# Kernel tuning notes

Hardware: AMD Instinct MI355X
Metric: run time of the kernel (lower is better)

Reference implementation:

```python
import jax, jax.numpy as jnp
import numpy as np

B, T, S = 64, 4096, 128


def setup_inputs() -> dict:
    key = jax.random.key(0)
    k1, k2 = jax.random.split(key)
    log_observation = jax.random.normal(k1, (B, T, S), dtype=jnp.float32)
    # a valid log-transition matrix (rows = from-state), all entries finite
    log_transition = jax.nn.log_softmax(jax.random.normal(k2, (S, S), dtype=jnp.float32), axis=1)
    return {"log_observation": log_observation, "log_transition": log_transition}


def reference(log_observation, log_transition):
    """CRF partition function (neg_log_likelihood_batch): -logsumexp over all paths.

    log_observation: [B, T, S], log_transition: [S, S] (from-state x to-state).
    Returns [B] negative log partition values.
    """
    obs_t = jnp.swapaxes(log_observation, 0, 1)  # [T, B, S] time-major for scan
    fv0 = obs_t[0]  # [B, S]

    def step(fv, obs):
        # (logsumexp, +) semiring recurrence: fv'[b,j] = LSE_i(fv[b,i] + A[i,j]) + obs[b,j]
        fv = jax.nn.logsumexp(fv[:, :, None] + log_transition[None], axis=1) + obs
        return fv, None

    fv, _ = jax.lax.scan(step, fv0, obs_t[1:])
    return -jax.nn.logsumexp(fv, axis=1)  # [B]
```

## Files before the change

kernel.cpp:

```cpp
#include <hip/hip_runtime.h>

typedef _Float16 half_t;
typedef _Float16 h8 __attribute__((ext_vector_type(8)));
typedef _Float16 h2 __attribute__((ext_vector_type(2)));
typedef float f4 __attribute__((ext_vector_type(4)));
typedef unsigned int uint32;
typedef unsigned long long u64;
typedef unsigned int u2v __attribute__((ext_vector_type(2)));

#define SHIFT16 2.772588722239781f
#define SHIFT8  2.0794415416798357f
#define WX 0
#define WQ 8192
#define WSC 16384
#define FAST_WS_BYTES 114688u

#define WAIT_VM(n)   asm volatile("s_waitcnt vmcnt(" #n ")" ::: "memory")

#define GL4(dst, addr, OFFSTR) \
    asm volatile("global_load_dwordx4 %0, %1, off offset:" OFFSTR \
                 : "=v"(dst) : "v"(addr))

__device__ __forceinline__ h2 pkrtz(float a, float b) {
    return __builtin_bit_cast(h2, __builtin_amdgcn_cvt_pkrtz(a, b));
}

__device__ __forceinline__ void swap32(uint32& a, uint32& b) {
#if __has_builtin(__builtin_amdgcn_permlane32_swap)
    u2v r = __builtin_amdgcn_permlane32_swap(a, b, false, false);
    a = r.x; b = r.y;
#else
    const uint32 pa = (uint32)__shfl_xor((int)a, 32);
    const uint32 pb = (uint32)__shfl_xor((int)b, 32);
    const bool hi = (threadIdx.x & 32) != 0;
    const uint32 na = hi ? pb : a;
    const uint32 nb = hi ? b : pa;
    a = na; b = nb;
#endif
}
__device__ __forceinline__ void swap16(uint32& a, uint32& b) {
#if __has_builtin(__builtin_amdgcn_permlane16_swap)
    u2v r = __builtin_amdgcn_permlane16_swap(a, b, false, false);
    a = r.x; b = r.y;
#else
    const uint32 sa = (uint32)__builtin_amdgcn_ds_swizzle((int)a, 0x401F);
    const uint32 sb = (uint32)__builtin_amdgcn_ds_swizzle((int)b, 0x401F);
    const bool m = (threadIdx.x & 16) != 0;
    const uint32 na = m ? sb : a;
    const uint32 nb = m ? b : sa;
    a = na; b = nb;
#endif
}

__device__ __forceinline__ float wavemax_hi(float M) {
    uint32 ma = __builtin_bit_cast(uint32, M), mb = ma;
    swap16(ma, mb);
    M = fmaxf(__builtin_bit_cast(float, ma), __builtin_bit_cast(float, mb));
    ma = __builtin_bit_cast(uint32, M); mb = ma;
    swap32(ma, mb);
    return fmaxf(__builtin_bit_cast(float, ma), __builtin_bit_cast(float, mb));
}

__device__ __forceinline__ float wavesum_hi(float S) {
    uint32 a = __builtin_bit_cast(uint32, S), b = a;
    swap16(a, b);
    S = __builtin_bit_cast(float, a) + __builtin_bit_cast(float, b);
    a = __builtin_bit_cast(uint32, S); b = a;
    swap32(a, b);
    return __builtin_bit_cast(float, a) + __builtin_bit_cast(float, b);
}

__device__ __forceinline__ float chain_sum(const f4 (&D)[8]) {
    f4 s4 = (D[0] + D[1]) + (D[2] + D[3]);
    s4 = s4 + ((D[4] + D[5]) + (D[6] + D[7]));
    float S = (s4.x + s4.y) + (s4.z + s4.w);
    return wavesum_hi(S);
}


#define TE(N) (FW ? (N) : (4095 - (N)))
#define WSEG 32
#define LSEG 64
#define NSEG 32

template <bool FW, int ST>
__device__ __forceinline__ void cstep(int v, int nv, bool head,
                                      f4 (&D)[8], const uint32 (&ep)[16],
                                      const h8 (&Af)[8][4],
                                      float& Lacc, float& rs, float& saK)
{
    const f4 Z = {0.f, 0.f, 0.f, 0.f};

    if (ST == 0) {
        #pragma unroll
        for (int mt = 0; mt < 8; ++mt) D[mt] = D[mt] * rs;
        if (v == WSEG) {
            if (head) {
                #pragma unroll
                for (int mt = 0; mt < 8; ++mt) D[mt] = (f4){1.f, 1.f, 1.f, 1.f};
            } else {
                saK = chain_sum(D);
            }
            Lacc = 0.f;
        }
    }
    if (ST == 3) {
        if (v != nv - 1) {
            f4 m01 = __builtin_elementwise_max(D[0], D[1]);
            f4 m23 = __builtin_elementwise_max(D[2], D[3]);
            f4 m45 = __builtin_elementwise_max(D[4], D[5]);
            f4 m67 = __builtin_elementwise_max(D[6], D[7]);
            f4 ma = __builtin_elementwise_max(
                        __builtin_elementwise_max(m01, m23),
                        __builtin_elementwise_max(m45, m67));
            float M = fmaxf(fmaxf(ma.x, ma.y), fmaxf(ma.z, ma.w));
            M = wavemax_hi(M);
            Lacc += __logf(M);
            rs = __builtin_amdgcn_rcpf(M);
        }
    }

    uint32 Wx[8], Wy[8];
    #pragma unroll
    for (int mt = 0; mt < 8; ++mt) {
        h2 w0 = pkrtz(D[mt].x, D[mt].y) * __builtin_bit_cast(h2, ep[2 * mt]);
        h2 w1 = pkrtz(D[mt].z, D[mt].w) * __builtin_bit_cast(h2, ep[2 * mt + 1]);
        Wx[mt] = __builtin_bit_cast(uint32, w0);
        Wy[mt] = __builtin_bit_cast(uint32, w1);
    }

    h8 Bf[4];
    #pragma unroll
    for (int kc = 0; kc < 4; ++kc) {
        uint32 x0 = Wx[2 * kc], x1 = Wx[2 * kc + 1];
        uint32 y0 = Wy[2 * kc], y1 = Wy[2 * kc + 1];
        swap32(x0, x1); swap16(x0, x1);
        swap32(y0, y1); swap16(y0, y1);
        uint4 bv; bv.x = x0; bv.y = y0; bv.z = x1; bv.w = y1;
        Bf[kc] = __builtin_bit_cast(h8, bv);
    }

    #pragma unroll
    for (int mt = 0; mt < 8; ++mt) {
        f4 acc = Z;
        acc = __builtin_amdgcn_mfma_f32_16x16x32_f16(Af[mt][0], Bf[0], acc, 0, 0, 0);
        acc = __builtin_amdgcn_mfma_f32_16x16x32_f16(Af[mt][1], Bf[1], acc, 0, 0, 0);
        acc = __builtin_amdgcn_mfma_f32_16x16x32_f16(Af[mt][2], Bf[2], acc, 0, 0, 0);
        acc = __builtin_amdgcn_mfma_f32_16x16x32_f16(Af[mt][3], Bf[3], acc, 0, 0, 0);
        D[mt] = acc;
    }
}

#define ISSUE8(B, IPE) do {                                                   \
    int ip_ = (IPE);                                                          \
    ip_ = ip_ < 0 ? 0 : (ip_ > NITd - 1 ? NITd - 1 : ip_);                    \
    const u64 a_ = lbase + ((u64)TE(ip_) << 9);                               \
    GL4(G[B][0], a_, "0");   GL4(G[B][1], a_, "64");                          \
    GL4(G[B][2], a_, "128"); GL4(G[B][3], a_, "192");                         \
    GL4(G[B][4], a_, "256"); GL4(G[B][5], a_, "320");                         \
    GL4(G[B][6], a_, "384"); GL4(G[B][7], a_, "448");                        \
} while (0)

#define SUBSTEP(U)  do {                                                      \
    const int v_ = tt * 8 + (U);                                              \
    if (v_ < nv) {                                                            \
        ISSUE8(((U) + 3) & 3, itb + v_ + 3);                                  \
        WAIT_VM(24);                             \
        __builtin_amdgcn_sched_barrier(0);                                    \
        uint32 ep[16];                                                        \
        _Pragma("unroll")                                                     \
        for (int mt = 0; mt < 8; ++mt) {                                      \
            const f4 ov = __builtin_bit_cast(f4, G[(U) & 3][mt]);             \
            ep[2 * mt] = __builtin_bit_cast(uint32,                           \
                pkrtz(__expf(ov.x - SHIFT16), __expf(ov.y - SHIFT16)));       \
            ep[2 * mt + 1] = __builtin_bit_cast(uint32,                       \
                pkrtz(__expf(ov.z - SHIFT16), __expf(ov.w - SHIFT16)));       \
        }                                                                     \
        cstep<FW, (U) & 3>(v_, nv, head, D, ep, Af, Lacc, rs, saK);           \
    } } while (0)

template <bool FW>
__device__ __forceinline__ void chain(const float* __restrict__ obs,
                                      const float* __restrict__ trans,
                                      float* __restrict__ ws, int cg, int sg)
{
    const int l = threadIdx.x & 63;
    const int q = l >> 4, n = l & 15;
    const int NITd = FW ? 2048 : 2047;
    const int nv   = (!FW && sg == NSEG - 1) ? (WSEG + LSEG - 1) : (WSEG + LSEG);
    const bool head = (sg == 0);
    const bool last = (sg == NSEG - 1);
    const int itb = sg * LSEG - WSEG;
    const u64 lbase = (u64)(const char*)obs
                    + ((u64)(cg * 16 + n) << 21)
                    + (u64)(q << 4);

    h8 Af[8][4];
    #pragma unroll
    for (int mt = 0; mt < 8; ++mt)
        #pragma unroll
        for (int kc = 0; kc < 4; ++kc) {
            h8 a;
            #pragma unroll
            for (int j = 0; j < 8; ++j) {
                const int k = kc * 32 + q * 8 + j;
                const int m = mt * 16 + n;
                a[j] = (half_t)__expf(FW ? trans[k * 128 + m] : trans[m * 128 + k]);
            }
            Af[mt][kc] = a;
        }

    uint4 G[4][8];
    ISSUE8(0, itb + 0);
    ISSUE8(1, itb + 1);
    ISSUE8(2, itb + 2);

    f4 D[8];
    #pragma unroll
    for (int mt = 0; mt < 8; ++mt) D[mt] = (f4){1.f, 1.f, 1.f, 1.f};
    float Lacc = 0.f, rs = 1.f, saK = 1.f;

    #pragma unroll 1
    for (int tt = 0; tt < (WSEG + LSEG) / 8; ++tt) {
        SUBSTEP(0); SUBSTEP(1); SUBSTEP(2); SUBSTEP(3);
        SUBSTEP(4); SUBSTEP(5); SUBSTEP(6); SUBSTEP(7);
    }
    WAIT_VM(0);

    const float swK = chain_sum(D);
    if (last) {
        float* Xo = ws + (FW ? WX : WQ) + ((cg * 16 + n) << 7);
        #pragma unroll
        for (int mt = 0; mt < 8; ++mt)
            *(f4*)&Xo[mt * 16 + q * 4] = D[mt];
    }
    float* sc = ws + WSC + (cg * 2 + (FW ? 0 : 1)) * 1536;
    if (q == 0) {
        sc[sg * 16 + n]        = Lacc;
        sc[512 + sg * 16 + n]  = swK;
        sc[1024 + sg * 16 + n] = head ? 1.0f : saK;
    }
}

__global__ __launch_bounds__(64, 1)
void crf_mfma(const float* __restrict__ obs, const float* __restrict__ trans,
              float* __restrict__ ws)
{
    const int bid = blockIdx.x;
    const int g = bid & 7;
    const int sg = bid >> 3;
    const int cg = g & 3;
    if (g < 4) chain<true >(obs, trans, ws, cg, sg);
    else       chain<false>(obs, trans, ws, cg, sg);
}

__global__ __launch_bounds__(64)
void crf_comb(const float* __restrict__ obs, const float* __restrict__ ws,
              float* __restrict__ out)
{
    const int b = blockIdx.x, l = threadIdx.x;
    const int cg = b >> 4, n = b & 15;
    const int s0 = 2 * l;
    const float2 o = *(const float2*)&obs[((((size_t)b << 12) + 2048) << 7) + s0];
    const float e0 = __expf(o.x - SHIFT16), e1 = __expf(o.y - SHIFT16);
    float v = ws[WX + b * 128 + s0] * e0 * ws[WQ + b * 128 + s0]
            + ws[WX + b * 128 + s0 + 1] * e1 * ws[WQ + b * 128 + s0 + 1];

    const int dir = l >> 5, s = l & 31;
    const float* sc = ws + WSC + (cg * 2 + dir) * 1536;
    float corr = sc[s * 16 + n];
    if (s >= 1)
        corr += __logf(sc[512 + (s - 1) * 16 + n])
              - __logf(sc[1024 + s * 16 + n]);

    v += __shfl_xor(v, 1);  v += __shfl_xor(v, 2);  v += __shfl_xor(v, 4);
    v += __shfl_xor(v, 8);  v += __shfl_xor(v, 16); v += __shfl_xor(v, 32);
    corr += __shfl_xor(corr, 1);  corr += __shfl_xor(corr, 2);
    corr += __shfl_xor(corr, 4);  corr += __shfl_xor(corr, 8);
    corr += __shfl_xor(corr, 16); corr += __shfl_xor(corr, 32);
    if (l == 0)
        out[b] = -(__logf(v) + corr + 4096.0f * SHIFT16);
}


typedef _Float16 h2f __attribute__((ext_vector_type(2)));
#define FTILE 16
#define FNTILE 128

#if __has_builtin(__builtin_amdgcn_fdot2)
#define FDOT2(p, e, acc) __builtin_amdgcn_fdot2((p), (e), (acc), false)
#else
#define FDOT2(p, e, acc) fmaf((float)(p).x, (float)(e).x, fmaf((float)(p).y, (float)(e).y, (acc)))
#endif

__device__ __forceinline__ h2f u2h(uint32 u) { return __builtin_bit_cast(h2f, u); }
__device__ __forceinline__ uint32 f2h(float f) {
    return (uint32)__builtin_bit_cast(unsigned short, (half_t)f);
}

#define FSTEP(N0, APPLY, MEAS)  do {                                                \
    const int row_ = fw ? ((N0) & (FTILE - 1)) : ((FTILE - 1) - ((N0) & (FTILE - 1))); \
    const float2 o2_ = *(const float2*)&obsL[(((N0) >> 4) & 1) * (FTILE * 128) + (row_ << 7) + (l << 1)]; \
    float e0_ = __expf(o2_.x - SHIFT8);                                             \
    float e1_ = __expf(o2_.y - SHIFT8);                                             \
    if (APPLY) { e0_ *= rsf; e1_ *= rsf; }                                          \
    float w0_, w1_;                                                                 \
    if (fw) { w0_ = pv0; w1_ = pv1; } else { w0_ = pv0 * e0_; w1_ = pv1 * e1_; }    \
    Pl[l] = (f2h(w1_) << 16) | f2h(w0_);                                            \
    float a0_=0.f,a1_=0.f,a2_=0.f,a3_=0.f,b0_=0.f,b1_=0.f,b2_=0.f,b3_=0.f;          \
    _Pragma("unroll")                                                               \
    for (int c_ = 0; c_ < 16; ++c_) {                                               \
        const uint4 q_ = ((const uint4*)Pl)[c_];                                    \
        const h2f p0_ = u2h(q_.x), p1_ = u2h(q_.y), p2_ = u2h(q_.z), p3_ = u2h(q_.w); \
        a0_ = FDOT2(p0_, eA[4*c_+0], a0_);                                          \
        a1_ = FDOT2(p1_, eA[4*c_+1], a1_);                                          \
        a2_ = FDOT2(p2_, eA[4*c_+2], a2_);                                          \
        a3_ = FDOT2(p3_, eA[4*c_+3], a3_);                                          \
        b0_ = FDOT2(p0_, eB[4*c_+0], b0_);                                          \
        b1_ = FDOT2(p1_, eB[4*c_+1], b1_);                                          \
        b2_ = FDOT2(p2_, eB[4*c_+2], b2_);                                          \
        b3_ = FDOT2(p3_, eB[4*c_+3], b3_);                                          \
    }                                                                               \
    const float s0_ = (a0_ + a1_) + (a2_ + a3_);                                    \
    const float s1_ = (b0_ + b1_) + (b2_ + b3_);                                    \
    if (fw) { pv0 = s0_ * e0_; pv1 = s1_ * e1_; } else { pv0 = s0_; pv1 = s1_; }    \
    if (MEAS) {                                                                     \
        float m_ = fmaxf(pv0, pv1);                                                 \
        m_ = fmaxf(m_, __shfl_xor(m_, 1));                                          \
        m_ = fmaxf(m_, __shfl_xor(m_, 2));                                          \
        m_ = fmaxf(m_, __shfl_xor(m_, 4));                                          \
        m_ = fmaxf(m_, __shfl_xor(m_, 8));                                          \
        m_ = fmaxf(m_, __shfl_xor(m_, 16));                                         \
        m_ = fmaxf(m_, __shfl_xor(m_, 32));                                         \
        rsf = __builtin_amdgcn_rcpf(m_);                                            \
        Lacc += __logf(m_);                                                         \
    }                                                                               \
} while (0)

#define FLOADR(TK) do {                                                             \
    const float4* g_ = (const float4*)(obsB + (size_t)(fw ? (TK) * (FTILE * 128)    \
                                      : (4096 - FTILE * ((TK) + 1)) * 128));        \
    r0 = g_[l];       r1 = g_[l + 64];  r2 = g_[l + 128]; r3 = g_[l + 192];         \
    r4 = g_[l + 256]; r5 = g_[l + 320]; r6 = g_[l + 384]; r7 = g_[l + 448];         \
} while (0)

#define FSTORER(TK) do {                                                            \
    float4* s_ = (float4*)&obsL[((TK) & 1) * (FTILE * 128)];                        \
    s_[l] = r0;       s_[l + 64] = r1;  s_[l + 128] = r2; s_[l + 192] = r3;         \
    s_[l + 256] = r4; s_[l + 320] = r5; s_[l + 384] = r6; s_[l + 448] = r7;         \
} while (0)

__global__ __launch_bounds__(64, 1)
void crf_half_fb(const float* __restrict__ obs, const float* __restrict__ trans,
                 float* __restrict__ ws)
{
    __shared__ __align__(16) uint32 Pl[64];
    __shared__ __align__(16) float obsL[2 * FTILE * 128];

    const int l  = threadIdx.x;
    const bool fw = blockIdx.x < 64;
    const int b  = fw ? blockIdx.x : blockIdx.x - 64;
    const float* obsB = obs + (size_t)b * 4096 * 128;

    h2f eA[64], eB[64];
    if (fw) {
        const int c0 = 2 * l;
        #pragma unroll
        for (int k = 0; k < 64; ++k) {
            h2f ta, tb;
            ta.x = (half_t)__expf(trans[(2*k    ) * 128 + c0]);
            ta.y = (half_t)__expf(trans[(2*k + 1) * 128 + c0]);
            tb.x = (half_t)__expf(trans[(2*k    ) * 128 + c0 + 1]);
            tb.y = (half_t)__expf(trans[(2*k + 1) * 128 + c0 + 1]);
            eA[k] = ta; eB[k] = tb;
        }
    } else {
        const int ro0 = (2 * l) * 128, ro1 = (2 * l + 1) * 128;
        #pragma unroll
        for (int k = 0; k < 64; ++k) {
            h2f ta, tb;
            ta.x = (half_t)__expf(trans[ro0 + 2*k]);
            ta.y = (half_t)__expf(trans[ro0 + 2*k + 1]);
            tb.x = (half_t)__expf(trans[ro1 + 2*k]);
            tb.y = (half_t)__expf(trans[ro1 + 2*k + 1]);
            eA[k] = ta; eB[k] = tb;
        }
    }

    float4 r0, r1, r2, r3, r4, r5, r6, r7;
    FLOADR(0);
    FSTORER(0);
    FLOADR(1);

    float rsf = 1.f, Lacc = 0.f, pv0, pv1;

    if (fw) {
        const float2 o2 = *(const float2*)&obsL[l << 1];
        pv0 = __expf(o2.x - SHIFT8);
        pv1 = __expf(o2.y - SHIFT8);
    } else {
        pv0 = 1.f; pv1 = 1.f;
        FSTEP(0, false, false);
    }

    for (int tile = 0; tile < FNTILE; ++tile) {
        if (tile > 0) {
            FSTORER(tile);
            if (tile < FNTILE - 1) FLOADR(tile + 1);
        }
        const int nb = tile << 4;
        #pragma unroll 1
        for (int g = 0; g < 4; ++g) {
            const int n0 = nb + (g << 2);
            if (n0 > 0) FSTEP(n0, true, false);
            FSTEP(n0 + 1, false, false);
            FSTEP(n0 + 2, false, false);
            if (n0 + 3 != 2047) FSTEP(n0 + 3, false, true);
            else                FSTEP(n0 + 3, false, false);
        }
    }

    if (fw) {
        ws[b * 128 + 2*l]     = pv0;
        ws[b * 128 + 2*l + 1] = pv1;
        if (l == 0) ws[16384 + b] = Lacc;
    } else {
        ws[8192 + b * 128 + 2*l]     = pv0;
        ws[8192 + b * 128 + 2*l + 1] = pv1;
        if (l == 0) ws[16448 + b] = Lacc;
    }
}

__global__ __launch_bounds__(64)
void crf_comb_fb(const float* __restrict__ ws, float* __restrict__ out)
{
    const int b = blockIdx.x, l = threadIdx.x;
    float s = ws[b * 128 + 2*l] * ws[8192 + b * 128 + 2*l]
            + ws[b * 128 + 2*l + 1] * ws[8192 + b * 128 + 2*l + 1];
    s += __shfl_xor(s, 1);  s += __shfl_xor(s, 2);  s += __shfl_xor(s, 4);
    s += __shfl_xor(s, 8);  s += __shfl_xor(s, 16); s += __shfl_xor(s, 32);
    if (l == 0)
        out[b] = -(__logf(s) + ws[16384 + b] + ws[16448 + b] + 4096.0f * SHIFT8);
}


extern "C" void kernel_launch(void* const* d_in, const int* in_sizes, int n_in,
                              void* d_out, int out_size, void* d_ws, size_t ws_size,
                              hipStream_t stream) {
    (void)in_sizes; (void)n_in; (void)out_size;
    const float* obs   = (const float*)d_in[0];
    const float* trans = (const float*)d_in[1];
    float* out = (float*)d_out;
    float* ws  = (float*)d_ws;

    if (ws_size >= (size_t)FAST_WS_BYTES) {
        hipLaunchKernelGGL(crf_mfma, dim3(256), dim3(64), 0, stream, obs, trans, ws);
        hipLaunchKernelGGL(crf_comb, dim3(64),  dim3(64), 0, stream, obs, ws, out);
    } else {
        hipLaunchKernelGGL(crf_half_fb, dim3(128), dim3(64), 0, stream, obs, trans, ws);
        hipLaunchKernelGGL(crf_comb_fb, dim3(64),  dim3(64), 0, stream, ws, out);
    }
}
```

Measured before the change: 243.3 us.

## Precompute fp16 exp(obs) in MFMA layout with a fully parallel prep kernel

```diff
diff --git a/kernel.cpp b/kernel.cpp
--- a/kernel.cpp
+++ b/kernel.cpp
@@ -14,6 +14,8 @@
 #define WQ 8192
 #define WSC 16384
 #define FAST_WS_BYTES 114688u
+#define EO2_OFF 131072u
+#define FAST2_WS_BYTES (EO2_OFF + 67108864u)
 
 #define WAIT_VM(n)   asm volatile("s_waitcnt vmcnt(" #n ")" ::: "memory")
 
@@ -85,7 +87,7 @@
 
 template <bool FW, int ST>
 __device__ __forceinline__ void cstep(int v, int nv, bool head,
-                                      f4 (&D)[8], const uint32 (&ep)[16],
+                                      f4 (&D)[8], const uint32* ep,
                                       const h8 (&Af)[8][4],
                                       float& Lacc, float& rs, float& saK)
 {
@@ -151,6 +153,144 @@
     }
 }
 
+#define AF_SETUP()                                                            \
+    h8 Af[8][4];                                                              \
+    _Pragma("unroll")                                                         \
+    for (int mt = 0; mt < 8; ++mt)                                            \
+        _Pragma("unroll")                                                     \
+        for (int kc = 0; kc < 4; ++kc) {                                      \
+            h8 a;                                                             \
+            _Pragma("unroll")                                                 \
+            for (int j = 0; j < 8; ++j) {                                     \
+                const int k = kc * 32 + q * 8 + j;                            \
+                const int m = mt * 16 + n;                                    \
+                a[j] = (half_t)__expf(FW ? trans[k * 128 + m]                 \
+                                         : trans[m * 128 + k]);               \
+            }                                                                 \
+            Af[mt][kc] = a;                                                   \
+        }
+
+#define EPILOGUE(DD, LACC, SAK)                                               \
+    const float swK = chain_sum(DD);                                          \
+    if (last) {                                                               \
+        float* Xo = ws + (FW ? WX : WQ) + ((cg * 16 + n) << 7);               \
+        _Pragma("unroll")                                                     \
+        for (int mt = 0; mt < 8; ++mt)                                        \
+            *(f4*)&Xo[mt * 16 + q * 4] = DD[mt];                              \
+    }                                                                         \
+    float* sc = ws + WSC + (cg * 2 + (FW ? 0 : 1)) * 1536;                    \
+    if (q == 0) {                                                             \
+        sc[sg * 16 + n]        = LACC;                                        \
+        sc[512 + sg * 16 + n]  = swK;                                         \
+        sc[1024 + sg * 16 + n] = head ? 1.0f : SAK;                           \
+    }
+
+
+__global__ __launch_bounds__(256)
+void eo_prep(const float* __restrict__ obs, uint32* __restrict__ eo)
+{
+    __shared__ float sb[64 * 130];
+    const int tid = threadIdx.x;
+    const int cg = blockIdx.x >> 10;
+    const int tb = blockIdx.x & 1023;
+
+    #pragma unroll
+    for (int i = 0; i < 8; ++i) {
+        const int idx = i * 256 + tid;
+        const int row = idx >> 5, c4 = idx & 31;
+        const int n = row >> 2, tl = row & 3;
+        const float4 v = *(const float4*)
+            &obs[((size_t)(cg * 16 + n) * 4096 + (tb * 4 + tl)) * 128 + c4 * 4];
+        *(float4*)&sb[row * 130 + c4 * 4] = v;
+    }
+    __syncthreads();
+
+    const int gg = tid >> 6;
+    const int l  = tid & 63;
+    const int q = l >> 4, nn = l & 15;
+    #pragma unroll
+    for (int tl = 0; tl < 4; ++tl) {
+        uint4 o;
+        uint32* po = &o.x;
+        #pragma unroll
+        for (int j = 0; j < 4; ++j) {
+            const int hd = gg * 4 + j;
+            const int mt = hd >> 1, rr = (hd & 1) * 2;
+            const int s = mt * 16 + q * 4 + rr;
+            const float* p = &sb[(nn * 4 + tl) * 130 + s];
+            po[j] = __builtin_bit_cast(uint32,
+                      pkrtz(__expf(p[0] - SHIFT16), __expf(p[1] - SHIFT16)));
+        }
+        *(uint4*)&eo[((size_t)(cg * 4096 + tb * 4 + tl) << 10) + (gg << 8) + (l << 2)] = o;
+    }
+}
+
+#define ISSUE4(B, IPE) do {                                                   \
+    int ip_ = (IPE);                                                          \
+    ip_ = ip_ < 0 ? 0 : (ip_ > NITd - 1 ? NITd - 1 : ip_);                    \
+    const u64 a_ = lbase + ((u64)TE(ip_) << 12);                              \
+    GL4(G[B][0], a_, "0");    GL4(G[B][1], a_, "1024");                       \
+    GL4(G[B][2], a_, "2048"); GL4(G[B][3], a_, "3072");                       \
+} while (0)
+
+#define ESUBSTEP(U)  do {                                                     \
+    const int v_ = tt * 8 + (U);                                              \
+    if (v_ < nv) {                                                            \
+        ISSUE4(((U) + 3) & 3, itb + v_ + 3);                                  \
+        WAIT_VM(12);                             \
+        __builtin_amdgcn_sched_barrier(0);                                    \
+        cstep<FW, (U) & 3>(v_, nv, head, D, (const uint32*)&G[(U) & 3][0],    \
+                           Af, Lacc, rs, saK);                                \
+    } } while (0)
+
+template <bool FW>
+__device__ __forceinline__ void chain_eo(const uint32* __restrict__ eo,
+                                         const float* __restrict__ trans,
+                                         float* __restrict__ ws, int cg, int sg)
+{
+    const int l = threadIdx.x & 63;
+    const int q = l >> 4, n = l & 15;
+    const int NITd = FW ? 2048 : 2047;
+    const int nv   = (!FW && sg == NSEG - 1) ? (WSEG + LSEG - 1) : (WSEG + LSEG);
+    const bool head = (sg == 0);
+    const bool last = (sg == NSEG - 1);
+    const int itb = sg * LSEG - WSEG;
+    const u64 lbase = (u64)(const char*)eo + ((u64)cg << 24) + (u64)(l << 4);
+
+    AF_SETUP();
+
+    uint4 G[4][4];
+    ISSUE4(0, itb + 0);
+    ISSUE4(1, itb + 1);
+    ISSUE4(2, itb + 2);
+
+    f4 D[8];
+    #pragma unroll
+    for (int mt = 0; mt < 8; ++mt) D[mt] = (f4){1.f, 1.f, 1.f, 1.f};
+    float Lacc = 0.f, rs = 1.f, saK = 1.f;
+
+    #pragma unroll 1
+    for (int tt = 0; tt < (WSEG + LSEG) / 8; ++tt) {
+        ESUBSTEP(0); ESUBSTEP(1); ESUBSTEP(2); ESUBSTEP(3);
+        ESUBSTEP(4); ESUBSTEP(5); ESUBSTEP(6); ESUBSTEP(7);
+    }
+    WAIT_VM(0);
+
+    EPILOGUE(D, Lacc, saK);
+}
+
+__global__ __launch_bounds__(64, 1)
+void crf_mfma_eo(const uint32* __restrict__ eo, const float* __restrict__ trans,
+                 float* __restrict__ ws)
+{
+    const int bid = blockIdx.x;
+    const int r = bid & 127;
+    const int cg = r >> 5, sg = r & 31;
+    if (bid < 128) chain_eo<true >(eo, trans, ws, cg, sg);
+    else           chain_eo<false>(eo, trans, ws, cg, sg);
+}
+
+
 #define ISSUE8(B, IPE) do {                                                   \
     int ip_ = (IPE);                                                          \
     ip_ = ip_ < 0 ? 0 : (ip_ > NITd - 1 ? NITd - 1 : ip_);                    \
@@ -158,7 +298,7 @@
     GL4(G[B][0], a_, "0");   GL4(G[B][1], a_, "64");                          \
     GL4(G[B][2], a_, "128"); GL4(G[B][3], a_, "192");                         \
     GL4(G[B][4], a_, "256"); GL4(G[B][5], a_, "320");                         \
-    GL4(G[B][6], a_, "384"); GL4(G[B][7], a_, "448");                        \
+    GL4(G[B][6], a_, "384"); GL4(G[B][7], a_, "448");                         \
 } while (0)
 
 #define SUBSTEP(U)  do {                                                      \
@@ -180,9 +320,9 @@
     } } while (0)
 
 template <bool FW>
-__device__ __forceinline__ void chain(const float* __restrict__ obs,
-                                      const float* __restrict__ trans,
-                                      float* __restrict__ ws, int cg, int sg)
+__device__ __forceinline__ void chain_g(const float* __restrict__ obs,
+                                        const float* __restrict__ trans,
+                                        float* __restrict__ ws, int cg, int sg)
 {
     const int l = threadIdx.x & 63;
     const int q = l >> 4, n = l & 15;
@@ -192,23 +332,9 @@
     const bool last = (sg == NSEG - 1);
     const int itb = sg * LSEG - WSEG;
     const u64 lbase = (u64)(const char*)obs
-                    + ((u64)(cg * 16 + n) << 21)
-                    + (u64)(q << 4);
-
-    h8 Af[8][4];
-    #pragma unroll
-    for (int mt = 0; mt < 8; ++mt)
-        #pragma unroll
-        for (int kc = 0; kc < 4; ++kc) {
-            h8 a;
-            #pragma unroll
-            for (int j = 0; j < 8; ++j) {
-                const int k = kc * 32 + q * 8 + j;
-                const int m = mt * 16 + n;
-                a[j] = (half_t)__expf(FW ? trans[k * 128 + m] : trans[m * 128 + k]);
-            }
-            Af[mt][kc] = a;
-        }
+                    + ((u64)(cg * 16 + n) << 21) + (u64)(q << 4);
+
+    AF_SETUP();
 
     uint4 G[4][8];
     ISSUE8(0, itb + 0);
@@ -227,31 +353,19 @@
     }
     WAIT_VM(0);
 
-    const float swK = chain_sum(D);
-    if (last) {
-        float* Xo = ws + (FW ? WX : WQ) + ((cg * 16 + n) << 7);
-        #pragma unroll
-        for (int mt = 0; mt < 8; ++mt)
-            *(f4*)&Xo[mt * 16 + q * 4] = D[mt];
-    }
-    float* sc = ws + WSC + (cg * 2 + (FW ? 0 : 1)) * 1536;
-    if (q == 0) {
-        sc[sg * 16 + n]        = Lacc;
-        sc[512 + sg * 16 + n]  = swK;
-        sc[1024 + sg * 16 + n] = head ? 1.0f : saK;
-    }
+    EPILOGUE(D, Lacc, saK);
 }
 
 __global__ __launch_bounds__(64, 1)
-void crf_mfma(const float* __restrict__ obs, const float* __restrict__ trans,
-              float* __restrict__ ws)
+void crf_mfma_g(const float* __restrict__ obs, const float* __restrict__ trans,
+                float* __restrict__ ws)
 {
     const int bid = blockIdx.x;
     const int g = bid & 7;
     const int sg = bid >> 3;
     const int cg = g & 3;
-    if (g < 4) chain<true >(obs, trans, ws, cg, sg);
-    else       chain<false>(obs, trans, ws, cg, sg);
+    if (g < 4) chain_g<true >(obs, trans, ws, cg, sg);
+    else       chain_g<false>(obs, trans, ws, cg, sg);
 }
 
 __global__ __launch_bounds__(64)
@@ -453,9 +567,14 @@
     float* out = (float*)d_out;
     float* ws  = (float*)d_ws;
 
-    if (ws_size >= (size_t)FAST_WS_BYTES) {
-        hipLaunchKernelGGL(crf_mfma, dim3(256), dim3(64), 0, stream, obs, trans, ws);
-        hipLaunchKernelGGL(crf_comb, dim3(64),  dim3(64), 0, stream, obs, ws, out);
+    if (ws_size >= (size_t)FAST2_WS_BYTES) {
+        uint32* eo = (uint32*)((char*)d_ws + EO2_OFF);
+        hipLaunchKernelGGL(eo_prep,     dim3(4096), dim3(256), 0, stream, obs, eo);
+        hipLaunchKernelGGL(crf_mfma_eo, dim3(256),  dim3(64),  0, stream, eo, trans, ws);
+        hipLaunchKernelGGL(crf_comb,    dim3(64),   dim3(64),  0, stream, obs, ws, out);
+    } else if (ws_size >= (size_t)FAST_WS_BYTES) {
+        hipLaunchKernelGGL(crf_mfma_g, dim3(256), dim3(64), 0, stream, obs, trans, ws);
+        hipLaunchKernelGGL(crf_comb,   dim3(64),  dim3(64), 0, stream, obs, ws, out);
     } else {
         hipLaunchKernelGGL(crf_half_fb, dim3(128), dim3(64), 0, stream, obs, trans, ws);
         hipLaunchKernelGGL(crf_comb_fb, dim3(64),  dim3(64), 0, stream, ws, out);
```

Result: no change. 241.7 us (-0.7%).
